# Kernel optimization log

Measured on AMD Instinct MI355X. Metric: run time of the kernel, lower is better.

Reference implementation:

```python
import jax, jax.numpy as jnp
import numpy as np

S, B, D, H, DH, E, F = 2048, 2, 512, 8, 64, 8, 1024
TOPK = 2


def setup_inputs() -> dict:
    key = jax.random.key(0)
    ks = jax.random.split(key, 12)
    rn = lambda k, shp, s=0.02: jax.random.normal(k, shp, jnp.float32) * s
    # RoPE tables (half-split convention): (S, DH)
    pos = jnp.arange(S, dtype=jnp.float32)[:, None]
    inv_freq = 1.0 / (10000.0 ** (jnp.arange(0, DH, 2, dtype=jnp.float32) / DH))
    ang = pos * inv_freq[None, :]                       # (S, DH//2)
    cos = jnp.concatenate([jnp.cos(ang), jnp.cos(ang)], axis=-1)
    sin = jnp.concatenate([jnp.sin(ang), jnp.sin(ang)], axis=-1)
    return {
        "src": jax.random.normal(ks[0], (S, B, D), jnp.float32),
        "cos": cos, "sin": sin,
        "Wq": rn(ks[1], (D, D)), "bq": jnp.zeros((D,), jnp.float32),
        "Wk": rn(ks[2], (D, D)), "bk": jnp.zeros((D,), jnp.float32),
        "Wv": rn(ks[3], (D, D)), "bv": jnp.zeros((D,), jnp.float32),
        "Wo": rn(ks[4], (D, D)), "bo": jnp.zeros((D,), jnp.float32),
        "ln1_g": jnp.ones((D,), jnp.float32), "ln1_b": jnp.zeros((D,), jnp.float32),
        "ln2_g": jnp.ones((D,), jnp.float32), "ln2_b": jnp.zeros((D,), jnp.float32),
        "Wg": rn(ks[5], (D, E)),
        "W1": rn(ks[6], (E, D, F)), "B1": jnp.zeros((E, F), jnp.float32),
        "W2": rn(ks[7], (E, F, D)), "B2": jnp.zeros((E, D), jnp.float32),
    }


def _layernorm(x, g, b, eps=1e-5):
    m = x.mean(-1, keepdims=True)
    v = ((x - m) ** 2).mean(-1, keepdims=True)
    return (x - m) * jax.lax.rsqrt(v + eps) * g + b


def _rotate_half(x):
    x1, x2 = jnp.split(x, 2, axis=-1)
    return jnp.concatenate([-x2, x1], axis=-1)


def _forward(src, cos, sin, Wq, bq, Wk, bk, Wv, bv, Wo, bo,
             ln1_g, ln1_b, ln2_g, ln2_b, Wg, W1, B1, W2, B2):
    # ---- RoPE self-attention ----
    q = (src @ Wq + bq).reshape(S, B, H, DH)
    k = (src @ Wk + bk).reshape(S, B, H, DH)
    v = (src @ Wv + bv).reshape(S, B, H, DH)
    c = cos[:, None, None, :]
    s = sin[:, None, None, :]
    q = q * c + _rotate_half(q) * s
    k = k * c + _rotate_half(k) * s
    scores = jnp.einsum("sbhd,tbhd->bhst", q, k) / jnp.sqrt(jnp.float32(DH))
    attn = jax.nn.softmax(scores, axis=-1)              # (B,H,S,S)
    ctx = jnp.einsum("bhst,tbhd->sbhd", attn, v).reshape(S, B, D)
    attn_out = ctx @ Wo + bo
    x = _layernorm(src + attn_out, ln1_g, ln1_b)
    # ---- MoE feed-forward (top-k softmax gating) ----
    xt = x.reshape(S * B, D)                            # (N, D)
    probs = jax.nn.softmax(xt @ Wg, axis=-1)            # (N, E)
    top_v, top_i = jax.lax.top_k(probs, TOPK)           # (N, TOPK)
    top_v = top_v / top_v.sum(-1, keepdims=True)
    N = S * B
    gates = jnp.zeros((N, E), jnp.float32).at[
        jnp.arange(N)[:, None], top_i].add(top_v)       # (N, E)
    h = jax.nn.relu(jnp.einsum("nd,edf->nef", xt, W1) + B1[None])   # (N,E,F)
    eo = jnp.einsum("nef,efd->ned", h, W2) + B2[None]               # (N,E,D)
    moe_out = jnp.einsum("ne,ned->nd", gates, eo).reshape(S, B, D)
    return _layernorm(x + moe_out, ln2_g, ln2_b)


def reference(src, cos, sin, Wq, bq, Wk, bk, Wv, bv, Wo, bo,
              ln1_g, ln1_b, ln2_g, ln2_b, Wg, W1, B1, W2, B2):
    return _forward(src, cos, sin, Wq, bq, Wk, bk, Wv, bv, Wo, bo,
                    ln1_g, ln1_b, ln2_g, ln2_b, Wg, W1, B1, W2, B2)
```

## Files before the change

### kernel.cpp

```cpp
#include <hip/hip_runtime.h>
#include <math.h>

#define S_  2048
#define B_  2
#define D_  512
#define H_  8
#define DH_ 64
#define E_  8
#define F_  1024
#define N_  4096
#define NPAIR_ 8192

typedef __attribute__((ext_vector_type(4))) float f32x4;
typedef __attribute__((ext_vector_type(8))) short short8;
typedef unsigned short u16;

__device__ __forceinline__ u16 f2bf(float f) {
  unsigned u = __builtin_bit_cast(unsigned, f);
  u += 0x7fffu + ((u >> 16) & 1u);
  return (u16)(u >> 16);
}
__device__ __forceinline__ float bf2f(u16 h) {
  unsigned u = ((unsigned)h) << 16;
  return __builtin_bit_cast(float, u);
}

__global__ __launch_bounds__(256) void src_split(const float* __restrict__ in,
                                                 u16* __restrict__ hi,
                                                 u16* __restrict__ lo) {
  size_t i = ((size_t)blockIdx.x * 256 + threadIdx.x) * 8;
  float f[8];
  *(float4*)&f[0] = *(const float4*)&in[i];
  *(float4*)&f[4] = *(const float4*)&in[i + 4];
  short8 h, l;
#pragma unroll
  for (int j = 0; j < 8; ++j) {
    u16 a = f2bf(f[j]);
    h[j] = (short)a;
    l[j] = (short)f2bf(f[j] - bf2f(a));
  }
  *(short8*)&hi[i] = h;
  *(short8*)&lo[i] = l;
}

__global__ __launch_bounds__(256) void wsplit_t(const float* __restrict__ W,
                                                u16* __restrict__ Whi,
                                                u16* __restrict__ Wlo,
                                                int Nn, int K) {
  __shared__ u16 Th[64][72];
  __shared__ u16 Tl[64][72];
  int kb = blockIdx.y * 64, nb = blockIdx.x * 64;
  int r = threadIdx.x >> 2, c0 = (threadIdx.x & 3) * 16;
  const float* wp = &W[(size_t)(kb + r) * Nn + nb + c0];
#pragma unroll
  for (int c = 0; c < 16; c += 4) {
    float4 t = *(const float4*)&wp[c];
    float f[4] = {t.x, t.y, t.z, t.w};
#pragma unroll
    for (int j = 0; j < 4; ++j) {
      u16 a = f2bf(f[j]);
      Th[r][c0 + c + j] = a;
      Tl[r][c0 + c + j] = f2bf(f[j] - bf2f(a));
    }
  }
  __syncthreads();
  short8 h0, h1, l0, l1;
#pragma unroll
  for (int j = 0; j < 8; ++j) {
    h0[j] = (short)Th[c0 + j][r];     h1[j] = (short)Th[c0 + 8 + j][r];
    l0[j] = (short)Tl[c0 + j][r];     l1[j] = (short)Tl[c0 + 8 + j][r];
  }
  size_t ob = (size_t)(nb + r) * K + kb + c0;
  *(short8*)&Whi[ob] = h0;  *(short8*)&Whi[ob + 8] = h1;
  *(short8*)&Wlo[ob] = l0;  *(short8*)&Wlo[ob + 8] = l1;
}

__global__ __launch_bounds__(256) void wtrans(const float* __restrict__ W,
                                              u16* __restrict__ Wt,
                                              int K, int Nn) {
  size_t eo = (size_t)blockIdx.z * K * Nn;
  __shared__ u16 T[64][72];
  int kb = blockIdx.y * 64, nb = blockIdx.x * 64;
  int r = threadIdx.x >> 2, c0 = (threadIdx.x & 3) * 16;
  const float* wp = &W[eo + (size_t)(kb + r) * Nn + nb + c0];
#pragma unroll
  for (int c = 0; c < 16; c += 4) {
    float4 t = *(const float4*)&wp[c];
    T[r][c0 + c + 0] = f2bf(t.x);
    T[r][c0 + c + 1] = f2bf(t.y);
    T[r][c0 + c + 2] = f2bf(t.z);
    T[r][c0 + c + 3] = f2bf(t.w);
  }
  __syncthreads();
  short8 s0, s1;
#pragma unroll
  for (int j = 0; j < 8; ++j) {
    s0[j] = (short)T[c0 + j][r];
    s1[j] = (short)T[c0 + 8 + j][r];
  }
  *(short8*)&Wt[eo + (size_t)(nb + r) * K + kb + c0] = s0;
  *(short8*)&Wt[eo + (size_t)(nb + r) * K + kb + c0 + 8] = s1;
}

__global__ __launch_bounds__(256) void qkv_mfma(const u16* __restrict__ Ah_g,
                                                const u16* __restrict__ Al_g,
                                                const u16* __restrict__ Bh_g,
                                                const u16* __restrict__ Bl_g,
                                                const float* __restrict__ bq,
                                                const float* __restrict__ bk,
                                                const float* __restrict__ bv,
                                                const float* __restrict__ cosb,
                                                const float* __restrict__ sinb,
                                                u16* __restrict__ qh, u16* __restrict__ ql,
                                                u16* __restrict__ kh, u16* __restrict__ kl,
                                                u16* __restrict__ vb) {
  __shared__ u16 Ah[128][40], Al[128][40], Bh[128][40], Bl[128][40];
  int tid = threadIdx.x;
  int w = tid >> 6, l = tid & 63;
  int wr = w >> 1, wc = w & 1;
  int lg = l >> 4, lx = l & 15;
  int m0 = blockIdx.x * 128, n0 = blockIdx.y * 128;
  int sr = tid >> 1, s16 = (tid & 1) * 16;
  const u16* Aph = Ah_g + (size_t)(m0 + sr) * 512;
  const u16* Apl = Al_g + (size_t)(m0 + sr) * 512;
  const u16* Bph = Bh_g + (size_t)(n0 + sr) * 512;
  const u16* Bpl = Bl_g + (size_t)(n0 + sr) * 512;
  f32x4 acc[4][4];
#pragma unroll
  for (int m = 0; m < 4; ++m)
#pragma unroll
    for (int n = 0; n < 4; ++n) acc[m][n] = (f32x4){0.f, 0.f, 0.f, 0.f};
  short8 ah0 = *(const short8*)&Aph[s16];
  short8 ah1 = *(const short8*)&Aph[s16 + 8];
  short8 al0 = *(const short8*)&Apl[s16];
  short8 al1 = *(const short8*)&Apl[s16 + 8];
  short8 bh0 = *(const short8*)&Bph[s16];
  short8 bh1 = *(const short8*)&Bph[s16 + 8];
  short8 bl0 = *(const short8*)&Bpl[s16];
  short8 bl1 = *(const short8*)&Bpl[s16 + 8];
  for (int k0 = 0; k0 < 512; k0 += 32) {
    __syncthreads();
    *(short8*)&Ah[sr][s16] = ah0; *(short8*)&Ah[sr][s16 + 8] = ah1;
    *(short8*)&Al[sr][s16] = al0; *(short8*)&Al[sr][s16 + 8] = al1;
    *(short8*)&Bh[sr][s16] = bh0; *(short8*)&Bh[sr][s16 + 8] = bh1;
    *(short8*)&Bl[sr][s16] = bl0; *(short8*)&Bl[sr][s16 + 8] = bl1;
    __syncthreads();
    if (k0 + 32 < 512) {
      int ko = k0 + 32 + s16;
      ah0 = *(const short8*)&Aph[ko]; ah1 = *(const short8*)&Aph[ko + 8];
      al0 = *(const short8*)&Apl[ko]; al1 = *(const short8*)&Apl[ko + 8];
      bh0 = *(const short8*)&Bph[ko]; bh1 = *(const short8*)&Bph[ko + 8];
      bl0 = *(const short8*)&Bpl[ko]; bl1 = *(const short8*)&Bpl[ko + 8];
    }
    short8 fah[4], fal[4], fbh[4], fbl[4];
#pragma unroll
    for (int m = 0; m < 4; ++m) {
      fah[m] = *(const short8*)&Ah[wr * 64 + m * 16 + lx][lg * 8];
      fal[m] = *(const short8*)&Al[wr * 64 + m * 16 + lx][lg * 8];
    }
#pragma unroll
    for (int n = 0; n < 4; ++n) {
      fbh[n] = *(const short8*)&Bh[wc * 64 + n * 16 + lx][lg * 8];
      fbl[n] = *(const short8*)&Bl[wc * 64 + n * 16 + lx][lg * 8];
    }
#pragma unroll
    for (int m = 0; m < 4; ++m)
#pragma unroll
      for (int n = 0; n < 4; ++n) {
        acc[m][n] = __builtin_amdgcn_mfma_f32_16x16x32_bf16(fah[m], fbh[n], acc[m][n], 0, 0, 0);
        acc[m][n] = __builtin_amdgcn_mfma_f32_16x16x32_bf16(fal[m], fbh[n], acc[m][n], 0, 0, 0);
        acc[m][n] = __builtin_amdgcn_mfma_f32_16x16x32_bf16(fah[m], fbl[n], acc[m][n], 0, 0, 0);
      }
  }
  int tcolbase = n0 + wc * 64;
  int tsel = tcolbase >> 9;
  int hbase = tcolbase & 511;
  const float* bias = (tsel == 0) ? bq : (tsel == 1) ? bk : bv;
  if (tsel == 2) {
#pragma unroll
    for (int m = 0; m < 4; ++m)
#pragma unroll
      for (int i = 0; i < 4; ++i) {
        int row = m0 + wr * 64 + m * 16 + lg * 4 + i;
#pragma unroll
        for (int n = 0; n < 4; ++n) {
          int col = hbase + n * 16 + lx;
          vb[(size_t)row * 512 + col] = f2bf(acc[m][n][i] + bias[col]);
        }
      }
  } else {
    u16* oh = tsel ? kh : qh;
    u16* ol = tsel ? kl : ql;
    float qsc = tsel ? 1.f : 0.125f;
#pragma unroll
    for (int m = 0; m < 4; ++m)
#pragma unroll
      for (int i = 0; i < 4; ++i) {
        int row = m0 + wr * 64 + m * 16 + lg * 4 + i;
        int s = row >> 1;
#pragma unroll
        for (int n = 0; n < 2; ++n) {
          int dln = n * 16 + lx;
          float c  = cosb[s * 64 + dln];
          float sn = sinb[s * 64 + dln];
          float a  = acc[m][n][i]     + bias[hbase + dln];
          float b2 = acc[m][n + 2][i] + bias[hbase + dln + 32];
          float ra = (a * c - b2 * sn) * qsc;
          float rb = (b2 * c + a * sn) * qsc;
          size_t ix = (size_t)row * 512 + hbase + dln;
          u16 rah = f2bf(ra);
          oh[ix] = rah; ol[ix] = f2bf(ra - bf2f(rah));
          u16 rbh = f2bf(rb);
          oh[ix + 32] = rbh; ol[ix + 32] = f2bf(rb - bf2f(rbh));
        }
      }
  }
}

__global__ __launch_bounds__(256) void attn_mfma2(const u16* __restrict__ qh,
                                                  const u16* __restrict__ ql,
                                                  const u16* __restrict__ kh,
                                                  const u16* __restrict__ kl,
                                                  const u16* __restrict__ vbuf,
                                                  u16* __restrict__ poh,
                                                  u16* __restrict__ pol,
                                                  float* __restrict__ pml) {
  __shared__ u16 Khi[64][72];
  __shared__ u16 Klo[64][72];
  __shared__ u16 Vt[64][72];
  __shared__ unsigned P2[4][16][32];
  int tid = threadIdx.x;
  int w = tid >> 6, l = tid & 63;
  int lg = l >> 4, lx = l & 15;
  int f = blockIdx.x;
  int xcd = f & 7, j = f >> 3;
  int slab = xcd + 8 * (j & 3);
  int qt = j >> 2;
  int bh = slab >> 1, kvh = slab & 1;
  int b = bh >> 3, h = bh & 7;

  short8 qfh[2], qfl[2];
  {
    int qrow = qt * 64 + w * 16 + lx;
    size_t qo = (size_t)(qrow * 2 + b) * 512 + h * 64 + lg * 8;
    qfh[0] = *(const short8*)&qh[qo];
    qfh[1] = *(const short8*)&qh[qo + 32];
    qfl[0] = *(const short8*)&ql[qo];
    qfl[1] = *(const short8*)&ql[qo + 32];
  }

  f32x4 o_acc[4];
#pragma unroll
  for (int dg = 0; dg < 4; ++dg) o_acc[dg] = (f32x4){0.f, 0.f, 0.f, 0.f};
  float m_run = -1e30f, l_run = 0.f;

  int kvr = tid >> 2, ds4 = (tid & 3) * 16;
  int kvc = tid & 63, dsg = (tid >> 6) * 16;
  int psw = (lx & 7) << 2;

  short8 rkh0, rkh1, rkl0, rkl1, rv0, rv1;
  {
    int t0 = kvh * 1024;
    size_t ko = (size_t)((t0 + kvr) * 2 + b) * 512 + h * 64 + ds4;
    rkh0 = *(const short8*)&kh[ko]; rkh1 = *(const short8*)&kh[ko + 8];
    rkl0 = *(const short8*)&kl[ko]; rkl1 = *(const short8*)&kl[ko + 8];
    size_t vo = (size_t)((t0 + kvc) * 2 + b) * 512 + h * 64 + dsg;
    rv0 = *(const short8*)&vbuf[vo]; rv1 = *(const short8*)&vbuf[vo + 8];
  }

  for (int tt = 0; tt < 1024; tt += 64) {
    __syncthreads();
    *(short8*)&Khi[kvr][ds4]     = rkh0;
    *(short8*)&Khi[kvr][ds4 + 8] = rkh1;
    *(short8*)&Klo[kvr][ds4]     = rkl0;
    *(short8*)&Klo[kvr][ds4 + 8] = rkl1;
#pragma unroll
    for (int c = 0; c < 8; ++c) {
      Vt[dsg + c][kvc] = (u16)rv0[c];
      Vt[dsg + 8 + c][kvc] = (u16)rv1[c];
    }
    __syncthreads();
    if (tt + 64 < 1024) {
      int t0 = kvh * 1024 + tt + 64;
      size_t ko = (size_t)((t0 + kvr) * 2 + b) * 512 + h * 64 + ds4;
      rkh0 = *(const short8*)&kh[ko]; rkh1 = *(const short8*)&kh[ko + 8];
      rkl0 = *(const short8*)&kl[ko]; rkl1 = *(const short8*)&kl[ko + 8];
      size_t vo = (size_t)((t0 + kvc) * 2 + b) * 512 + h * 64 + dsg;
      rv0 = *(const short8*)&vbuf[vo]; rv1 = *(const short8*)&vbuf[vo + 8];
    }

    f32x4 sc[4];
#pragma unroll
    for (int cg = 0; cg < 4; ++cg) {
      short8 kf0 = *(const short8*)&Khi[cg * 16 + lx][lg * 8];
      short8 kf1 = *(const short8*)&Khi[cg * 16 + lx][32 + lg * 8];
      short8 kg0 = *(const short8*)&Klo[cg * 16 + lx][lg * 8];
      short8 kg1 = *(const short8*)&Klo[cg * 16 + lx][32 + lg * 8];
      f32x4 a = (f32x4){0.f, 0.f, 0.f, 0.f};
      a = __builtin_amdgcn_mfma_f32_16x16x32_bf16(kf0, qfh[0], a, 0, 0, 0);
      a = __builtin_amdgcn_mfma_f32_16x16x32_bf16(kf1, qfh[1], a, 0, 0, 0);
      a = __builtin_amdgcn_mfma_f32_16x16x32_bf16(kf0, qfl[0], a, 0, 0, 0);
      a = __builtin_amdgcn_mfma_f32_16x16x32_bf16(kf1, qfl[1], a, 0, 0, 0);
      a = __builtin_amdgcn_mfma_f32_16x16x32_bf16(kg0, qfh[0], a, 0, 0, 0);
      a = __builtin_amdgcn_mfma_f32_16x16x32_bf16(kg1, qfh[1], a, 0, 0, 0);
      sc[cg] = a;
    }

    float tm = sc[0][0];
#pragma unroll
    for (int cg = 0; cg < 4; ++cg)
#pragma unroll
      for (int i = 0; i < 4; ++i) tm = fmaxf(tm, sc[cg][i]);
    tm = fmaxf(tm, __shfl_xor(tm, 16));
    tm = fmaxf(tm, __shfl_xor(tm, 32));
    float mn = fmaxf(m_run, tm);
    float corr = __expf(m_run - mn);
    m_run = mn;
    float ts = 0.f;
#pragma unroll
    for (int cg = 0; cg < 4; ++cg)
#pragma unroll
      for (int i = 0; i < 4; ++i) {
        float pv = __expf(sc[cg][i] - mn);
        sc[cg][i] = pv;
        ts += pv;
      }
    ts += __shfl_xor(ts, 16);
    ts += __shfl_xor(ts, 32);
    l_run = l_run * corr + ts;
#pragma unroll
    for (int dg = 0; dg < 4; ++dg) o_acc[dg] *= corr;

#pragma unroll
    for (int cg = 0; cg < 4; ++cg)
#pragma unroll
      for (int t = 0; t < 2; ++t) {
        unsigned dw = (unsigned)f2bf(sc[cg][2 * t]) |
                      ((unsigned)f2bf(sc[cg][2 * t + 1]) << 16);
        P2[w][lx][(8 * cg + 2 * lg + t) ^ psw] = dw;
      }
    short8 pf0 = *(const short8*)&P2[w][lx][(4 * lg) ^ psw];
    short8 pf1 = *(const short8*)&P2[w][lx][(16 + 4 * lg) ^ psw];

#pragma unroll
    for (int dg = 0; dg < 4; ++dg) {
      short8 v0 = *(const short8*)&Vt[dg * 16 + lx][lg * 8];
      short8 v1 = *(const short8*)&Vt[dg * 16 + lx][32 + lg * 8];
      o_acc[dg] = __builtin_amdgcn_mfma_f32_16x16x32_bf16(v0, pf0, o_acc[dg], 0, 0, 0);
      o_acc[dg] = __builtin_amdgcn_mfma_f32_16x16x32_bf16(v1, pf1, o_acc[dg], 0, 0, 0);
    }
  }

  {
    int qrow = qt * 64 + w * 16 + lx;
    int row2 = qrow * 2 + b;
    size_t base = (size_t)kvh * ((size_t)N_ * D_) + (size_t)row2 * 512 + h * 64;
#pragma unroll
    for (int dg = 0; dg < 4; ++dg)
#pragma unroll
      for (int i = 0; i < 4; ++i) {
        int d = dg * 16 + 4 * lg + i;
        float val = o_acc[dg][i];
        u16 hi = f2bf(val);
        poh[base + d] = hi;
        pol[base + d] = f2bf(val - bf2f(hi));
      }
    if (lg == 0) {
      int u = row2 * 8 + h;
      pml[(size_t)kvh * 65536 + u * 2 + 0] = m_run;
      pml[(size_t)kvh * 65536 + u * 2 + 1] = l_run;
    }
  }
}

__global__ __launch_bounds__(256) void merge_attn2(const u16* __restrict__ poh,
                                                   const u16* __restrict__ pol,
                                                   const float* __restrict__ pml,
                                                   u16* __restrict__ ch,
                                                   u16* __restrict__ cl) {
  int u = blockIdx.x * 4 + (threadIdx.x >> 6);
  int lane = threadIdx.x & 63;
  float m0 = pml[u * 2], l0 = pml[u * 2 + 1];
  float m1 = pml[65536 + u * 2], l1 = pml[65536 + u * 2 + 1];
  float m = fmaxf(m0, m1);
  float e0 = __expf(m0 - m), e1 = __expf(m1 - m);
  float inv = 1.f / (l0 * e0 + l1 * e1);
  int n = u >> 3, h = u & 7;
  size_t base = (size_t)n * 512 + h * 64 + lane;
  const size_t PO1 = (size_t)N_ * D_;
  float v0 = bf2f(poh[base]) + bf2f(pol[base]);
  float v1 = bf2f(poh[PO1 + base]) + bf2f(pol[PO1 + base]);
  float val = (v0 * e0 + v1 * e1) * inv;
  u16 hi = f2bf(val);
  ch[base] = hi;
  cl[base] = f2bf(val - bf2f(hi));
}

__global__ __launch_bounds__(256) void wo_mfma(const u16* __restrict__ Ah_g,
                                               const u16* __restrict__ Al_g,
                                               const u16* __restrict__ Bh_g,
                                               const u16* __restrict__ Bl_g,
                                               const float* __restrict__ bias,
                                               float* __restrict__ C) {
  __shared__ u16 Ah[128][40], Al[128][40], Bh[128][40], Bl[128][40];
  int tid = threadIdx.x;
  int w = tid >> 6, l = tid & 63;
  int wr = w >> 1, wc = w & 1;
  int lg = l >> 4, lx = l & 15;
  int m0 = blockIdx.x * 128, n0 = blockIdx.y * 128;
  int sr = tid >> 1, s16 = (tid & 1) * 16;
  const u16* Aph = Ah_g + (size_t)(m0 + sr) * 512;
  const u16* Apl = Al_g + (size_t)(m0 + sr) * 512;
  const u16* Bph = Bh_g + (size_t)(n0 + sr) * 512;
  const u16* Bpl = Bl_g + (size_t)(n0 + sr) * 512;
  f32x4 acc[4][4];
#pragma unroll
  for (int m = 0; m < 4; ++m)
#pragma unroll
    for (int n = 0; n < 4; ++n) acc[m][n] = (f32x4){0.f, 0.f, 0.f, 0.f};
  short8 ah0 = *(const short8*)&Aph[s16];
  short8 ah1 = *(const short8*)&Aph[s16 + 8];
  short8 al0 = *(const short8*)&Apl[s16];
  short8 al1 = *(const short8*)&Apl[s16 + 8];
  short8 bh0 = *(const short8*)&Bph[s16];
  short8 bh1 = *(const short8*)&Bph[s16 + 8];
  short8 bl0 = *(const short8*)&Bpl[s16];
  short8 bl1 = *(const short8*)&Bpl[s16 + 8];
  for (int k0 = 0; k0 < 512; k0 += 32) {
    __syncthreads();
    *(short8*)&Ah[sr][s16] = ah0; *(short8*)&Ah[sr][s16 + 8] = ah1;
    *(short8*)&Al[sr][s16] = al0; *(short8*)&Al[sr][s16 + 8] = al1;
    *(short8*)&Bh[sr][s16] = bh0; *(short8*)&Bh[sr][s16 + 8] = bh1;
    *(short8*)&Bl[sr][s16] = bl0; *(short8*)&Bl[sr][s16 + 8] = bl1;
    __syncthreads();
    if (k0 + 32 < 512) {
      int ko = k0 + 32 + s16;
      ah0 = *(const short8*)&Aph[ko]; ah1 = *(const short8*)&Aph[ko + 8];
      al0 = *(const short8*)&Apl[ko]; al1 = *(const short8*)&Apl[ko + 8];
      bh0 = *(const short8*)&Bph[ko]; bh1 = *(const short8*)&Bph[ko + 8];
      bl0 = *(const short8*)&Bpl[ko]; bl1 = *(const short8*)&Bpl[ko + 8];
    }
    short8 fah[4], fal[4], fbh[4], fbl[4];
#pragma unroll
    for (int m = 0; m < 4; ++m) {
      fah[m] = *(const short8*)&Ah[wr * 64 + m * 16 + lx][lg * 8];
      fal[m] = *(const short8*)&Al[wr * 64 + m * 16 + lx][lg * 8];
    }
#pragma unroll
    for (int n = 0; n < 4; ++n) {
      fbh[n] = *(const short8*)&Bh[wc * 64 + n * 16 + lx][lg * 8];
      fbl[n] = *(const short8*)&Bl[wc * 64 + n * 16 + lx][lg * 8];
    }
#pragma unroll
    for (int m = 0; m < 4; ++m)
#pragma unroll
      for (int n = 0; n < 4; ++n) {
        acc[m][n] = __builtin_amdgcn_mfma_f32_16x16x32_bf16(fah[m], fbh[n], acc[m][n], 0, 0, 0);
        acc[m][n] = __builtin_amdgcn_mfma_f32_16x16x32_bf16(fal[m], fbh[n], acc[m][n], 0, 0, 0);
        acc[m][n] = __builtin_amdgcn_mfma_f32_16x16x32_bf16(fah[m], fbl[n], acc[m][n], 0, 0, 0);
      }
  }
#pragma unroll
  for (int m = 0; m < 4; ++m)
#pragma unroll
    for (int i = 0; i < 4; ++i) {
      int row = m0 + wr * 64 + m * 16 + lg * 4 + i;
#pragma unroll
      for (int n = 0; n < 4; ++n) {
        int col = n0 + wc * 64 + n * 16 + lx;
        C[(size_t)row * 512 + col] = acc[m][n][i] + bias[col];
      }
    }
}

__global__ __launch_bounds__(256) void ln_res(const float* __restrict__ a,
                                              const float* __restrict__ b,
                                              const float* __restrict__ g,
                                              const float* __restrict__ beta,
                                              float* __restrict__ out,
                                              u16* __restrict__ obf) {
  int n = blockIdx.x * 4 + (threadIdx.x >> 6);
  int lane = threadIdx.x & 63;
  float v[8];
  float s = 0.f;
#pragma unroll
  for (int i = 0; i < 8; ++i) {
    int d = lane + 64 * i;
    v[i] = a[(size_t)n * D_ + d] + b[(size_t)n * D_ + d];
    s += v[i];
  }
#pragma unroll
  for (int m = 32; m; m >>= 1) s += __shfl_xor(s, m);
  float mean = s * (1.f / D_);
  float s2 = 0.f;
#pragma unroll
  for (int i = 0; i < 8; ++i) { float t = v[i] - mean; s2 += t * t; }
#pragma unroll
  for (int m = 32; m; m >>= 1) s2 += __shfl_xor(s2, m);
  float r = rsqrtf(s2 * (1.f / D_) + 1e-5f);
#pragma unroll
  for (int i = 0; i < 8; ++i) {
    int d = lane + 64 * i;
    float val = (v[i] - mean) * r * g[d] + beta[d];
    out[(size_t)n * D_ + d] = val;
    obf[(size_t)n * D_ + d] = f2bf(val);
  }
}

__global__ __launch_bounds__(256) void ln2_final(const float* __restrict__ x,
                                                 const u16* __restrict__ mp,
                                                 const float* __restrict__ g,
                                                 const float* __restrict__ beta,
                                                 float* __restrict__ out) {
  int n = blockIdx.x * 4 + (threadIdx.x >> 6);
  int lane = threadIdx.x & 63;
  float v[8];
  float s = 0.f;
#pragma unroll
  for (int i = 0; i < 8; ++i) {
    int d = lane + 64 * i;
    v[i] = x[(size_t)n * D_ + d] + bf2f(mp[(size_t)(2 * n) * D_ + d]) +
           bf2f(mp[(size_t)(2 * n + 1) * D_ + d]);
    s += v[i];
  }
#pragma unroll
  for (int m = 32; m; m >>= 1) s += __shfl_xor(s, m);
  float mean = s * (1.f / D_);
  float s2 = 0.f;
#pragma unroll
  for (int i = 0; i < 8; ++i) { float t = v[i] - mean; s2 += t * t; }
#pragma unroll
  for (int m = 32; m; m >>= 1) s2 += __shfl_xor(s2, m);
  float r = rsqrtf(s2 * (1.f / D_) + 1e-5f);
#pragma unroll
  for (int i = 0; i < 8; ++i) {
    int d = lane + 64 * i;
    out[(size_t)n * D_ + d] = (v[i] - mean) * r * g[d] + beta[d];
  }
}

__global__ __launch_bounds__(256) void gate_compute(const float* __restrict__ x,
                                                    const float* __restrict__ Wg,
                                                    float* __restrict__ gp,
                                                    int* __restrict__ tope) {
  int n = blockIdx.x * 4 + (threadIdx.x >> 6);
  int lane = threadIdx.x & 63;
  float p[E_] = {};
  for (int d = lane; d < D_; d += 64) {
    float xv = x[(size_t)n * D_ + d];
    const float* wr = &Wg[(size_t)d * E_];
#pragma unroll
    for (int e = 0; e < E_; ++e) p[e] += xv * wr[e];
  }
#pragma unroll
  for (int e = 0; e < E_; ++e)
#pragma unroll
    for (int m = 32; m; m >>= 1) p[e] += __shfl_xor(p[e], m);
  if (lane == 0) {
    float mx = p[0];
#pragma unroll
    for (int e = 1; e < E_; ++e) mx = fmaxf(mx, p[e]);
    float q[E_];
#pragma unroll
    for (int e = 0; e < E_; ++e) q[e] = expf(p[e] - mx);
    int e1 = 0;
#pragma unroll
    for (int e = 1; e < E_; ++e) if (q[e] > q[e1]) e1 = e;
    int e2 = (e1 == 0) ? 1 : 0;
#pragma unroll
    for (int e = 0; e < E_; ++e) if (e != e1 && q[e] > q[e2]) e2 = e;
    float denom = q[e1] + q[e2];
    gp[n * 2] = q[e1] / denom;
    gp[n * 2 + 1] = q[e2] / denom;
    tope[n] = e1 | (e2 << 8);
  }
}

__global__ __launch_bounds__(256) void route_build(const int* __restrict__ tope,
                                                   int* __restrict__ cnt,
                                                   int* __restrict__ lst) {
  int e = blockIdx.x;
  __shared__ int wsum[4];
  __shared__ int basem;
  int tid = threadIdx.x;
  int w = tid >> 6, lane = tid & 63;
  if (tid == 0) basem = 0;
  __syncthreads();
  for (int c0 = 0; c0 < N_; c0 += 256) {
    int n = c0 + tid;
    int te = tope[n];
    int e1 = te & 0xff, e2 = (te >> 8) & 0xff;
    bool m2 = (e2 == e);
    bool flag = (e1 == e) || m2;
    unsigned long long mask = __ballot(flag);
    int wpre = __popcll(mask & ((1ull << lane) - 1ull));
    if (lane == 0) wsum[w] = __popcll(mask);
    __syncthreads();
    int woff = 0;
    for (int i = 0; i < w; ++i) woff += wsum[i];
    int total = wsum[0] + wsum[1] + wsum[2] + wsum[3];
    if (flag) lst[e * N_ + basem + woff + wpre] = n * 2 + (m2 ? 1 : 0);
    __syncthreads();
    if (tid == 0) basem += total;
    __syncthreads();
  }
  if (tid == 0) cnt[e] = basem;
}

template <int MODE>
__global__ __launch_bounds__(256) void moe_mfma(const u16* __restrict__ Abase,
                                                const u16* __restrict__ Wt,
                                                const float* __restrict__ bias,
                                                const float* __restrict__ gp,
                                                u16* __restrict__ outp,
                                                const int* __restrict__ cnt,
                                                const int* __restrict__ lst) {
  constexpr int K  = MODE ? 1024 : 512;
  constexpr int Nn = MODE ? 512 : 1024;
  constexpr int NT = Nn / 128;
  constexpr int NI = K / 32;
  int fidx = blockIdx.x;
  int e = fidx & 7;
  int r = fidx >> 3;
  int nt = r % NT;
  int mt = r / NT;
  int c = cnt[e];
  int m0 = mt * 64;
  if (m0 >= c) return;
  int off = 0;
#pragma unroll
  for (int i = 0; i < E_; ++i) if (i < e) off += cnt[i];
  int n0 = nt * 128;
  __shared__ u16 As[64][40];
  __shared__ u16 Bs[128][40];
  int tid = threadIdx.x;
  int w = tid >> 6, l = tid & 63;
  int lg = l >> 4, lx = l & 15;
  int arow = tid >> 2, aseg = (tid & 3) * 8;
  int brow = tid >> 1, bseg = (tid & 1) * 16;
  int ar = m0 + arow; if (ar >= c) ar = c - 1;
  const u16* Ap;
  if (MODE == 0) Ap = Abase + (size_t)(lst[e * N_ + ar] >> 1) * 512 + aseg;
  else           Ap = Abase + (size_t)(off + ar) * 1024 + aseg;
  const u16* Bp = Wt + (size_t)e * K * Nn + (size_t)(n0 + brow) * K + bseg;

  f32x4 acc[4][2];
#pragma unroll
  for (int m = 0; m < 4; ++m)
#pragma unroll
    for (int n = 0; n < 2; ++n) acc[m][n] = (f32x4){0.f, 0.f, 0.f, 0.f};

  short8 pa  = *(const short8*)&Ap[0];
  short8 pb0 = *(const short8*)&Bp[0];
  short8 pb1 = *(const short8*)&Bp[8];
  for (int kk = 0; kk < NI; ++kk) {
    __syncthreads();
    *(short8*)&As[arow][aseg] = pa;
    *(short8*)&Bs[brow][bseg] = pb0;
    *(short8*)&Bs[brow][bseg + 8] = pb1;
    __syncthreads();
    if (kk + 1 < NI) {
      int ko = (kk + 1) * 32;
      pa  = *(const short8*)&Ap[ko];
      pb0 = *(const short8*)&Bp[ko];
      pb1 = *(const short8*)&Bp[ko + 8];
    }
    short8 af[4], bf[2];
#pragma unroll
    for (int m = 0; m < 4; ++m)
      af[m] = *(const short8*)&As[m * 16 + lx][lg * 8];
#pragma unroll
    for (int n = 0; n < 2; ++n)
      bf[n] = *(const short8*)&Bs[w * 32 + n * 16 + lx][lg * 8];
#pragma unroll
    for (int m = 0; m < 4; ++m)
#pragma unroll
      for (int n = 0; n < 2; ++n)
        acc[m][n] = __builtin_amdgcn_mfma_f32_16x16x32_bf16(af[m], bf[n], acc[m][n], 0, 0, 0);
  }
#pragma unroll
  for (int m = 0; m < 4; ++m)
#pragma unroll
    for (int i = 0; i < 4; ++i) {
      int rr = m0 + m * 16 + lg * 4 + i;
      if (rr < c) {
#pragma unroll
        for (int n = 0; n < 2; ++n) {
          int col = n0 + w * 32 + n * 16 + lx;
          float val = acc[m][n][i] + bias[e * Nn + col];
          if (MODE == 0) {
            outp[(size_t)(off + rr) * 1024 + col] = f2bf(fmaxf(val, 0.f));
          } else {
            int p = lst[e * N_ + rr];
            outp[(size_t)p * 512 + col] = f2bf(gp[p] * val);
          }
        }
      }
    }
}

extern "C" void kernel_launch(void* const* d_in, const int* in_sizes, int n_in,
                              void* d_out, int out_size, void* d_ws, size_t ws_size,
                              hipStream_t stream) {
  const float* src  = (const float*)d_in[0];
  const float* cosb = (const float*)d_in[1];
  const float* sinb = (const float*)d_in[2];
  const float* Wq   = (const float*)d_in[3];
  const float* bq   = (const float*)d_in[4];
  const float* Wk   = (const float*)d_in[5];
  const float* bk   = (const float*)d_in[6];
  const float* Wv   = (const float*)d_in[7];
  const float* bv   = (const float*)d_in[8];
  const float* Wo   = (const float*)d_in[9];
  const float* bo   = (const float*)d_in[10];
  const float* ln1g = (const float*)d_in[11];
  const float* ln1b = (const float*)d_in[12];
  const float* ln2g = (const float*)d_in[13];
  const float* ln2b = (const float*)d_in[14];
  const float* Wg   = (const float*)d_in[15];
  const float* W1   = (const float*)d_in[16];
  const float* B1   = (const float*)d_in[17];
  const float* W2   = (const float*)d_in[18];
  const float* B2   = (const float*)d_in[19];
  float* out = (float*)d_out;
  char* wsb = (char*)d_ws;

  const size_t MB1 = 1u << 20;
  u16* sh   = (u16*)(wsb + 0 * MB1);
  u16* sl   = (u16*)(wsb + 4 * MB1);
  u16* qhb  = (u16*)(wsb + 8 * MB1);
  u16* qlb  = (u16*)(wsb + 12 * MB1);
  u16* khb  = (u16*)(wsb + 16 * MB1);
  u16* klb  = (u16*)(wsb + 20 * MB1);
  u16* vbuf = (u16*)(wsb + 24 * MB1);
  u16* poh  = (u16*)(wsb + 28 * MB1);
  u16* pol  = (u16*)(wsb + 36 * MB1);
  float* pml = (float*)(wsb + 44 * MB1);
  float* aob = (float*)(wsb + 28 * MB1);
  float* xb  = (float*)(wsb + 36 * MB1);
  u16* xbf   = (u16*)(wsb + 44 * MB1);
  u16* Wqkv_hi = (u16*)(wsb + 48 * MB1);
  u16* Wqkv_lo = (u16*)(wsb + 48 * MB1 + 1572864);
  u16* Wo_hi   = (u16*)(wsb + 48 * MB1 + 3145728);
  u16* Wo_lo   = (u16*)(wsb + 48 * MB1 + 3670016);
  u16* W1t     = (u16*)(wsb + 52 * MB1);
  u16* W2t     = (u16*)(wsb + 28 * MB1);
  float* gpb   = (float*)(wsb + 60 * MB1);
  int* cnt     = (int*)(wsb + 60 * MB1 + 32768);
  int* lst     = (int*)(wsb + 60 * MB1 + 32768 + 64);
  int* tope    = (int*)(wsb + 60 * MB1 + 32768 + 64 + 131072);
  u16* ch  = sh;
  u16* cl  = sl;
  u16* hbf = (u16*)(wsb + 8 * MB1);
  u16* mp  = (u16*)(wsb + 0 * MB1);

  dim3 blk(256);
  src_split<<<dim3(1024), blk, 0, stream>>>(src, sh, sl);
  wsplit_t<<<dim3(8, 8), blk, 0, stream>>>(Wq, Wqkv_hi, Wqkv_lo, 512, 512);
  wsplit_t<<<dim3(8, 8), blk, 0, stream>>>(Wk, Wqkv_hi + 512 * 512, Wqkv_lo + 512 * 512, 512, 512);
  wsplit_t<<<dim3(8, 8), blk, 0, stream>>>(Wv, Wqkv_hi + 1024 * 512, Wqkv_lo + 1024 * 512, 512, 512);
  wsplit_t<<<dim3(8, 8), blk, 0, stream>>>(Wo, Wo_hi, Wo_lo, 512, 512);
  qkv_mfma<<<dim3(32, 12), blk, 0, stream>>>(sh, sl, Wqkv_hi, Wqkv_lo, bq, bk, bv,
                                             cosb, sinb, qhb, qlb, khb, klb, vbuf);
  attn_mfma2<<<dim3(1024), blk, 0, stream>>>(qhb, qlb, khb, klb, vbuf, poh, pol, pml);
  merge_attn2<<<dim3(8192), blk, 0, stream>>>(poh, pol, pml, ch, cl);
  wo_mfma<<<dim3(32, 4), blk, 0, stream>>>(ch, cl, Wo_hi, Wo_lo, bo, aob);
  ln_res<<<dim3(1024), blk, 0, stream>>>(src, aob, ln1g, ln1b, xb, xbf);
  wtrans<<<dim3(8, 16, 8), blk, 0, stream>>>(W2, W2t, 1024, 512);
  wtrans<<<dim3(16, 8, 8), blk, 0, stream>>>(W1, W1t, 512, 1024);
  gate_compute<<<dim3(1024), blk, 0, stream>>>(xb, Wg, gpb, tope);
  route_build<<<dim3(8), blk, 0, stream>>>(tope, cnt, lst);
  moe_mfma<0><<<dim3(8 * 8 * 64), blk, 0, stream>>>(xbf, W1t, B1, gpb, hbf, cnt, lst);
  moe_mfma<1><<<dim3(8 * 4 * 64), blk, 0, stream>>>(hbf, W2t, B2, gpb, mp, cnt, lst);
  ln2_final<<<dim3(1024), blk, 0, stream>>>(xb, mp, ln2g, ln2b, out);
}
```

Before: 237.8 us.

## Enlarge attention and MoE GEMM tiles, fuse gating into first layernorm

The attention kernel now uses 512-thread blocks covering 128 query rows, so each K/V tile loaded into shared memory serves twice as many queries and half as many blocks are launched. The MoE GEMM moves from 64x128 to 128x128 tiles with a 2x2 wave layout and 4x4 MFMA accumulators per wave, raising reuse per shared-memory load. The gate softmax/top-2 computation is folded into the post-attention layernorm kernel, removing one launch and a reread of x. Costs: more registers per thread in MoE, more padded work for experts whose token count is not a multiple of 128, and fewer blocks for load balancing.

```diff
diff --git a/kernel.cpp b/kernel.cpp
--- a/kernel.cpp
+++ b/kernel.cpp
@@ -217,7 +217,7 @@
   }
 }
 
-__global__ __launch_bounds__(256) void attn_mfma2(const u16* __restrict__ qh,
+__global__ __launch_bounds__(512) void attn_mfma2(const u16* __restrict__ qh,
                                                   const u16* __restrict__ ql,
                                                   const u16* __restrict__ kh,
                                                   const u16* __restrict__ kl,
@@ -228,7 +228,7 @@
   __shared__ u16 Khi[64][72];
   __shared__ u16 Klo[64][72];
   __shared__ u16 Vt[64][72];
-  __shared__ unsigned P2[4][16][32];
+  __shared__ unsigned P2[8][16][32];
   int tid = threadIdx.x;
   int w = tid >> 6, l = tid & 63;
   int lg = l >> 4, lx = l & 15;
@@ -241,7 +241,7 @@
 
   short8 qfh[2], qfl[2];
   {
-    int qrow = qt * 64 + w * 16 + lx;
+    int qrow = qt * 128 + w * 16 + lx;
     size_t qo = (size_t)(qrow * 2 + b) * 512 + h * 64 + lg * 8;
     qfh[0] = *(const short8*)&qh[qo];
     qfh[1] = *(const short8*)&qh[qo + 32];
@@ -254,39 +254,34 @@
   for (int dg = 0; dg < 4; ++dg) o_acc[dg] = (f32x4){0.f, 0.f, 0.f, 0.f};
   float m_run = -1e30f, l_run = 0.f;
 
-  int kvr = tid >> 2, ds4 = (tid & 3) * 16;
-  int kvc = tid & 63, dsg = (tid >> 6) * 16;
+  int kvr = tid >> 3, ds4 = (tid & 7) * 8;
+  int kvc = tid & 63, dsg = (tid >> 6) * 8;
   int psw = (lx & 7) << 2;
 
-  short8 rkh0, rkh1, rkl0, rkl1, rv0, rv1;
+  short8 rkh, rkl, rv;
   {
     int t0 = kvh * 1024;
     size_t ko = (size_t)((t0 + kvr) * 2 + b) * 512 + h * 64 + ds4;
-    rkh0 = *(const short8*)&kh[ko]; rkh1 = *(const short8*)&kh[ko + 8];
-    rkl0 = *(const short8*)&kl[ko]; rkl1 = *(const short8*)&kl[ko + 8];
+    rkh = *(const short8*)&kh[ko];
+    rkl = *(const short8*)&kl[ko];
     size_t vo = (size_t)((t0 + kvc) * 2 + b) * 512 + h * 64 + dsg;
-    rv0 = *(const short8*)&vbuf[vo]; rv1 = *(const short8*)&vbuf[vo + 8];
+    rv = *(const short8*)&vbuf[vo];
   }
 
   for (int tt = 0; tt < 1024; tt += 64) {
     __syncthreads();
-    *(short8*)&Khi[kvr][ds4]     = rkh0;
-    *(short8*)&Khi[kvr][ds4 + 8] = rkh1;
-    *(short8*)&Klo[kvr][ds4]     = rkl0;
-    *(short8*)&Klo[kvr][ds4 + 8] = rkl1;
-#pragma unroll
-    for (int c = 0; c < 8; ++c) {
-      Vt[dsg + c][kvc] = (u16)rv0[c];
-      Vt[dsg + 8 + c][kvc] = (u16)rv1[c];
-    }
+    *(short8*)&Khi[kvr][ds4] = rkh;
+    *(short8*)&Klo[kvr][ds4] = rkl;
+#pragma unroll
+    for (int c = 0; c < 8; ++c) Vt[dsg + c][kvc] = (u16)rv[c];
     __syncthreads();
     if (tt + 64 < 1024) {
       int t0 = kvh * 1024 + tt + 64;
       size_t ko = (size_t)((t0 + kvr) * 2 + b) * 512 + h * 64 + ds4;
-      rkh0 = *(const short8*)&kh[ko]; rkh1 = *(const short8*)&kh[ko + 8];
-      rkl0 = *(const short8*)&kl[ko]; rkl1 = *(const short8*)&kl[ko + 8];
+      rkh = *(const short8*)&kh[ko];
+      rkl = *(const short8*)&kl[ko];
       size_t vo = (size_t)((t0 + kvc) * 2 + b) * 512 + h * 64 + dsg;
-      rv0 = *(const short8*)&vbuf[vo]; rv1 = *(const short8*)&vbuf[vo + 8];
+      rv = *(const short8*)&vbuf[vo];
     }
 
     f32x4 sc[4];
@@ -352,7 +347,7 @@
   }
 
   {
-    int qrow = qt * 64 + w * 16 + lx;
+    int qrow = qt * 128 + w * 16 + lx;
     int row2 = qrow * 2 + b;
     size_t base = (size_t)kvh * ((size_t)N_ * D_) + (size_t)row2 * 512 + h * 64;
 #pragma unroll
@@ -473,12 +468,15 @@
     }
 }
 
-__global__ __launch_bounds__(256) void ln_res(const float* __restrict__ a,
-                                              const float* __restrict__ b,
-                                              const float* __restrict__ g,
-                                              const float* __restrict__ beta,
-                                              float* __restrict__ out,
-                                              u16* __restrict__ obf) {
+__global__ __launch_bounds__(256) void ln_res_gate(const float* __restrict__ a,
+                                                   const float* __restrict__ b,
+                                                   const float* __restrict__ g,
+                                                   const float* __restrict__ beta,
+                                                   const float* __restrict__ Wg,
+                                                   float* __restrict__ out,
+                                                   u16* __restrict__ obf,
+                                                   float* __restrict__ gp,
+                                                   int* __restrict__ tope) {
   int n = blockIdx.x * 4 + (threadIdx.x >> 6);
   int lane = threadIdx.x & 63;
   float v[8];
@@ -498,12 +496,38 @@
 #pragma unroll
   for (int m = 32; m; m >>= 1) s2 += __shfl_xor(s2, m);
   float r = rsqrtf(s2 * (1.f / D_) + 1e-5f);
+  float p[E_] = {};
 #pragma unroll
   for (int i = 0; i < 8; ++i) {
     int d = lane + 64 * i;
     float val = (v[i] - mean) * r * g[d] + beta[d];
     out[(size_t)n * D_ + d] = val;
     obf[(size_t)n * D_ + d] = f2bf(val);
+    const float* wr = &Wg[(size_t)d * E_];
+#pragma unroll
+    for (int e = 0; e < E_; ++e) p[e] += val * wr[e];
+  }
+#pragma unroll
+  for (int e = 0; e < E_; ++e)
+#pragma unroll
+    for (int m = 32; m; m >>= 1) p[e] += __shfl_xor(p[e], m);
+  if (lane == 0) {
+    float mx = p[0];
+#pragma unroll
+    for (int e = 1; e < E_; ++e) mx = fmaxf(mx, p[e]);
+    float q[E_];
+#pragma unroll
+    for (int e = 0; e < E_; ++e) q[e] = expf(p[e] - mx);
+    int e1 = 0;
+#pragma unroll
+    for (int e = 1; e < E_; ++e) if (q[e] > q[e1]) e1 = e;
+    int e2 = (e1 == 0) ? 1 : 0;
+#pragma unroll
+    for (int e = 0; e < E_; ++e) if (e != e1 && q[e] > q[e2]) e2 = e;
+    float denom = q[e1] + q[e2];
+    gp[n * 2] = q[e1] / denom;
+    gp[n * 2 + 1] = q[e2] / denom;
+    tope[n] = e1 | (e2 << 8);
   }
 }
 
@@ -536,43 +560,6 @@
   for (int i = 0; i < 8; ++i) {
     int d = lane + 64 * i;
     out[(size_t)n * D_ + d] = (v[i] - mean) * r * g[d] + beta[d];
-  }
-}
-
-__global__ __launch_bounds__(256) void gate_compute(const float* __restrict__ x,
-                                                    const float* __restrict__ Wg,
-                                                    float* __restrict__ gp,
-                                                    int* __restrict__ tope) {
-  int n = blockIdx.x * 4 + (threadIdx.x >> 6);
-  int lane = threadIdx.x & 63;
-  float p[E_] = {};
-  for (int d = lane; d < D_; d += 64) {
-    float xv = x[(size_t)n * D_ + d];
-    const float* wr = &Wg[(size_t)d * E_];
-#pragma unroll
-    for (int e = 0; e < E_; ++e) p[e] += xv * wr[e];
-  }
-#pragma unroll
-  for (int e = 0; e < E_; ++e)
-#pragma unroll
-    for (int m = 32; m; m >>= 1) p[e] += __shfl_xor(p[e], m);
-  if (lane == 0) {
-    float mx = p[0];
-#pragma unroll
-    for (int e = 1; e < E_; ++e) mx = fmaxf(mx, p[e]);
-    float q[E_];
-#pragma unroll
-    for (int e = 0; e < E_; ++e) q[e] = expf(p[e] - mx);
-    int e1 = 0;
-#pragma unroll
-    for (int e = 1; e < E_; ++e) if (q[e] > q[e1]) e1 = e;
-    int e2 = (e1 == 0) ? 1 : 0;
-#pragma unroll
-    for (int e = 0; e < E_; ++e) if (e != e1 && q[e] > q[e2]) e2 = e;
-    float denom = q[e1] + q[e2];
-    gp[n * 2] = q[e1] / denom;
-    gp[n * 2 + 1] = q[e2] / denom;
-    tope[n] = e1 | (e2 << 8);
   }
 }
 
@@ -625,68 +612,71 @@
   int nt = r % NT;
   int mt = r / NT;
   int c = cnt[e];
-  int m0 = mt * 64;
+  int m0 = mt * 128;
   if (m0 >= c) return;
   int off = 0;
 #pragma unroll
   for (int i = 0; i < E_; ++i) if (i < e) off += cnt[i];
   int n0 = nt * 128;
-  __shared__ u16 As[64][40];
+  __shared__ u16 As[128][40];
   __shared__ u16 Bs[128][40];
   int tid = threadIdx.x;
   int w = tid >> 6, l = tid & 63;
+  int wr = w >> 1, wc = w & 1;
   int lg = l >> 4, lx = l & 15;
-  int arow = tid >> 2, aseg = (tid & 3) * 8;
-  int brow = tid >> 1, bseg = (tid & 1) * 16;
-  int ar = m0 + arow; if (ar >= c) ar = c - 1;
+  int sr = tid >> 1, s16 = (tid & 1) * 16;
+  int ar = m0 + sr; if (ar >= c) ar = c - 1;
   const u16* Ap;
-  if (MODE == 0) Ap = Abase + (size_t)(lst[e * N_ + ar] >> 1) * 512 + aseg;
-  else           Ap = Abase + (size_t)(off + ar) * 1024 + aseg;
-  const u16* Bp = Wt + (size_t)e * K * Nn + (size_t)(n0 + brow) * K + bseg;
-
-  f32x4 acc[4][2];
+  if (MODE == 0) Ap = Abase + (size_t)(lst[e * N_ + ar] >> 1) * 512;
+  else           Ap = Abase + (size_t)(off + ar) * 1024;
+  const u16* Bp = Wt + (size_t)e * K * Nn + (size_t)(n0 + sr) * K;
+
+  f32x4 acc[4][4];
 #pragma unroll
   for (int m = 0; m < 4; ++m)
 #pragma unroll
-    for (int n = 0; n < 2; ++n) acc[m][n] = (f32x4){0.f, 0.f, 0.f, 0.f};
-
-  short8 pa  = *(const short8*)&Ap[0];
-  short8 pb0 = *(const short8*)&Bp[0];
-  short8 pb1 = *(const short8*)&Bp[8];
+    for (int n = 0; n < 4; ++n) acc[m][n] = (f32x4){0.f, 0.f, 0.f, 0.f};
+
+  short8 pa0 = *(const short8*)&Ap[s16];
+  short8 pa1 = *(const short8*)&Ap[s16 + 8];
+  short8 pb0 = *(const short8*)&Bp[s16];
+  short8 pb1 = *(const short8*)&Bp[s16 + 8];
   for (int kk = 0; kk < NI; ++kk) {
     __syncthreads();
-    *(short8*)&As[arow][aseg] = pa;
-    *(short8*)&Bs[brow][bseg] = pb0;
-    *(short8*)&Bs[brow][bseg + 8] = pb1;
+    *(short8*)&As[sr][s16] = pa0;
+    *(short8*)&As[sr][s16 + 8] = pa1;
+    *(short8*)&Bs[sr][s16] = pb0;
+    *(short8*)&Bs[sr][s16 + 8] = pb1;
     __syncthreads();
     if (kk + 1 < NI) {
-      int ko = (kk + 1) * 32;
-      pa  = *(const short8*)&Ap[ko];
+      int ko = (kk + 1) * 32 + s16;
+      pa0 = *(const short8*)&Ap[ko];
+      pa1 = *(const short8*)&Ap[ko + 8];
       pb0 = *(const short8*)&Bp[ko];
       pb1 = *(const short8*)&Bp[ko + 8];
     }
-    short8 af[4], bf[2];
+    short8 a[4], bfr[4];
 #pragma unroll
     for (int m = 0; m < 4; ++m)
-      af[m] = *(const short8*)&As[m * 16 + lx][lg * 8];
-#pragma unroll
-    for (int n = 0; n < 2; ++n)
-      bf[n] = *(const short8*)&Bs[w * 32 + n * 16 + lx][lg * 8];
+      a[m] = *(const short8*)&As[wr * 64 + m * 16 + lx][lg * 8];
+#pragma unroll
+    for (int n = 0; n < 4; ++n)
+      bfr[n] = *(const short8*)&Bs[wc * 64 + n * 16 + lx][lg * 8];
 #pragma unroll
     for (int m = 0; m < 4; ++m)
 #pragma unroll
-      for (int n = 0; n < 2; ++n)
-        acc[m][n] = __builtin_amdgcn_mfma_f32_16x16x32_bf16(af[m], bf[n], acc[m][n], 0, 0, 0);
+      for (int n = 0; n < 4; ++n)
+        acc[m][n] = __builtin_amdgcn_mfma_f32_16x16x32_bf16(a[m], bfr[n], acc[m][n], 0, 0, 0);
   }
 #pragma unroll
   for (int m = 0; m < 4; ++m)
 #pragma unroll
-    for (int i = 0; i < 4; ++i) {
-      int rr = m0 + m * 16 + lg * 4 + i;
-      if (rr < c) {
-#pragma unroll
-        for (int n = 0; n < 2; ++n) {
-          int col = n0 + w * 32 + n * 16 + lx;
+    for (int n = 0; n < 4; ++n)
+#pragma unroll
+      for (int i = 0; i < 4; ++i) {
+        int rr = m0 + wr * 64 + m * 16 + lg * 4 + i;
+        if (rr < c) {
+          int col = n0 + wc * 64 + n * 16 + lx;
           float val = acc[m][n][i] + bias[e * Nn + col];
           if (MODE == 0) {
             outp[(size_t)(off + rr) * 1024 + col] = f2bf(fmaxf(val, 0.f));
@@ -696,7 +686,6 @@
           }
         }
       }
-    }
 }
 
 extern "C" void kernel_launch(void* const* d_in, const int* in_sizes, int n_in,
@@ -762,15 +751,14 @@
   wsplit_t<<<dim3(8, 8), blk, 0, stream>>>(Wo, Wo_hi, Wo_lo, 512, 512);
   qkv_mfma<<<dim3(32, 12), blk, 0, stream>>>(sh, sl, Wqkv_hi, Wqkv_lo, bq, bk, bv,
                                              cosb, sinb, qhb, qlb, khb, klb, vbuf);
-  attn_mfma2<<<dim3(1024), blk, 0, stream>>>(qhb, qlb, khb, klb, vbuf, poh, pol, pml);
+  attn_mfma2<<<dim3(512), dim3(512), 0, stream>>>(qhb, qlb, khb, klb, vbuf, poh, pol, pml);
   merge_attn2<<<dim3(8192), blk, 0, stream>>>(poh, pol, pml, ch, cl);
   wo_mfma<<<dim3(32, 4), blk, 0, stream>>>(ch, cl, Wo_hi, Wo_lo, bo, aob);
-  ln_res<<<dim3(1024), blk, 0, stream>>>(src, aob, ln1g, ln1b, xb, xbf);
+  ln_res_gate<<<dim3(1024), blk, 0, stream>>>(src, aob, ln1g, ln1b, Wg, xb, xbf, gpb, tope);
   wtrans<<<dim3(8, 16, 8), blk, 0, stream>>>(W2, W2t, 1024, 512);
   wtrans<<<dim3(16, 8, 8), blk, 0, stream>>>(W1, W1t, 512, 1024);
-  gate_compute<<<dim3(1024), blk, 0, stream>>>(xb, Wg, gpb, tope);
   route_build<<<dim3(8), blk, 0, stream>>>(tope, cnt, lst);
-  moe_mfma<0><<<dim3(8 * 8 * 64), blk, 0, stream>>>(xbf, W1t, B1, gpb, hbf, cnt, lst);
-  moe_mfma<1><<<dim3(8 * 4 * 64), blk, 0, stream>>>(hbf, W2t, B2, gpb, mp, cnt, lst);
+  moe_mfma<0><<<dim3(8 * 8 * 32), blk, 0, stream>>>(xbf, W1t, B1, gpb, hbf, cnt, lst);
+  moe_mfma<1><<<dim3(8 * 4 * 32), blk, 0, stream>>>(hbf, W2t, B2, gpb, mp, cnt, lst);
   ln2_final<<<dim3(1024), blk, 0, stream>>>(xb, mp, ln2g, ln2b, out);
 }
```

After: 257.0 us. 1.08x slower.
